# Performance work log

Hardware: AMD Instinct MI355X
Metric: run time of the kernel (lower is better)

## Reference

```python
import jax, jax.numpy as jnp
import numpy as np
import math

EPS = 1e-07
ITERATIONS = 3
FINAL_LAMBDA = 0.01

B, H, W, K, CIN, COUT, P = 8, 12, 12, 3, 16, 32, 16


def setup_inputs() -> dict:
    key = jax.random.key(0)
    k1, k2, k3, k4 = jax.random.split(key, 4)
    V = jax.random.normal(k1, (B, H, W, K, K, CIN, COUT, P), dtype=jnp.float32)
    a = jax.random.uniform(k2, (B, H, W, K, K, CIN, 1), dtype=jnp.float32)
    Beta_u = jax.random.normal(k3, (1, 1, 1, 1, 1, 1, COUT, 1), dtype=jnp.float32)
    Beta_a = jax.random.normal(k4, (1, 1, 1, 1, 1, 1, COUT), dtype=jnp.float32)
    R = jnp.full((B, H, W, K, K, CIN, COUT), 1.0 / COUT, dtype=jnp.float32)
    outSize = (B, H, W, COUT, P)
    return {"V": V, "a": a, "Beta_u": Beta_u, "Beta_a": Beta_a, "R": R, "outSize": outSize}


def _l2_normalize(x, axis):
    n = jnp.sqrt(jnp.sum(x * x, axis=axis, keepdims=True))
    return x / jnp.maximum(n, 1e-12)  # matches F.normalize default eps


def reference(V, a, Beta_u, Beta_a, R, outSize):
    mathpilog = jnp.log(jnp.asarray(2.0 * math.pi, dtype=jnp.float32))
    mu = sigma_sqr = a_out = None
    for i in range(ITERATIONS):
        Lam = FINAL_LAMBDA * (1.0 - 0.95 ** (i + 1))
        Rw = (R * a)[..., None]                                  # [B,h,w,K,K,Cin,Cout,1]
        mu_denom = jnp.sum(Rw, axis=(3, 4, 5), keepdims=True)    # [B,h,w,1,1,1,Cout,1]
        mu = jnp.sum(Rw * V, axis=(3, 4, 5), keepdims=True) / (mu_denom + EPS)  # [B,h,w,1,1,1,Cout,P]
        V_mu_sqr = (V - mu) ** 2                                 # [B,h,w,K,K,Cin,Cout,P]
        sigma_sqr = jnp.sum(Rw * V_mu_sqr, axis=(3, 4, 5), keepdims=True) / (mu_denom + EPS)
        cost_h = (Beta_u + 0.5 * jnp.log(sigma_sqr)) * mu_denom  # [B,h,w,1,1,1,Cout,P]
        x = Lam * (Beta_a - jnp.sum(cost_h, axis=7))             # [B,h,w,1,1,1,Cout]
        a_out = jax.nn.sigmoid(_l2_normalize(x, axis=6))
        log_p1 = -0.5 * jnp.sum(mathpilog + jnp.log(sigma_sqr), axis=7) + EPS
        log_p2 = -jnp.sum(V_mu_sqr / (2.0 * sigma_sqr + EPS), axis=7)  # [B,h,w,K,K,Cin,Cout]
        R = jax.nn.softmax(jnp.log(a_out) + log_p1 + log_p2, axis=6)
    mu_out = jnp.squeeze(mu).reshape(outSize)
    sigma_out = jnp.squeeze(sigma_sqr).reshape(outSize)
    return mu_out, jnp.squeeze(a_out), sigma_out
```

## Files before the change

### kernel.cpp

```cpp
#include <hip/hip_runtime.h>
#include <math.h>

#define NPOS 1152
#define NN   144
#define COUT 32
#define PP   16
#define EPSF 1e-7f
#define LOG2PI 1.8378770664093453f

#define MU_OFF   0
#define A_OFF    589824
#define SIG_OFF  626688

__global__ void __launch_bounds__(256)
em_routing_kernel(const float* __restrict__ V,
                  const float* __restrict__ a,
                  const float* __restrict__ Bu,
                  const float* __restrict__ Ba,
                  const float* __restrict__ Rin,
                  float* __restrict__ out)
{
    const int pos  = blockIdx.x;
    const int tid  = threadIdx.x;
    const int c    = tid & 31;
    const int slot = tid >> 5;
    const int wave = tid >> 6;

    const float* Vp = V + (size_t)pos * (NN * COUT * PP);
    const float* Rp = Rin + (size_t)pos * (NN * COUT);

    __shared__ float a_s[NN];
    __shared__ float red[4][COUT][33];
    __shared__ float fin[COUT][33];
    __shared__ float mu_s[COUT][17];
    __shared__ float wp_s[COUT][17];
    __shared__ float sg_s[COUT][17];
    __shared__ float cl_s[COUT];
    __shared__ float xs[COUT];
    __shared__ float sl_s[COUT];
    __shared__ float ao_s[COUT];
    __shared__ float nrm_s;

    for (int i = tid; i < NN; i += 256) a_s[i] = a[pos * NN + i];
    __syncthreads();

    const float lam_tab[3] = {0.01f * (1.f - 0.95f),
                              0.01f * (1.f - 0.95f * 0.95f),
                              0.01f * (1.f - 0.95f * 0.95f * 0.95f)};

    float mu_r[PP], wp_r[PP];
    float cl_r = 0.f;

    for (int it = 0; it < 3; ++it) {
        if (it > 0) {
            #pragma unroll
            for (int p = 0; p < PP; ++p) {
                mu_r[p] = mu_s[c][p];
                wp_r[p] = wp_s[c][p];
            }
            cl_r = cl_s[c];
        }

        float S0 = 0.f, S1[PP], S2[PP];
        #pragma unroll
        for (int p = 0; p < PP; ++p) { S1[p] = 0.f; S2[p] = 0.f; }

        for (int j = 0; j < 18; ++j) {
            const int n = slot + (j << 3);
            const float4* vp = (const float4*)(Vp + (size_t)n * (COUT * PP) + c * PP);
            float4 q0 = vp[0], q1 = vp[1], q2 = vp[2], q3 = vp[3];
            float v[PP] = {q0.x,q0.y,q0.z,q0.w, q1.x,q1.y,q1.z,q1.w,
                           q2.x,q2.y,q2.z,q2.w, q3.x,q3.y,q3.z,q3.w};
            float Rw;
            if (it == 0) {
                Rw = Rp[n * COUT + c] * a_s[n];
            } else {
                float acc = 0.f;
                #pragma unroll
                for (int p = 0; p < PP; ++p) {
                    float d = v[p] - mu_r[p];
                    acc = fmaf(d * wp_r[p], d, acc);
                }
                float logit = cl_r - acc;
                float m = logit;
                #pragma unroll
                for (int msk = 1; msk <= 16; msk <<= 1)
                    m = fmaxf(m, __shfl_xor(m, msk, 64));
                float e = __expf(logit - m);
                float sum = e;
                #pragma unroll
                for (int msk = 1; msk <= 16; msk <<= 1)
                    sum += __shfl_xor(sum, msk, 64);
                Rw = (e / sum) * a_s[n];
            }
            S0 += Rw;
            #pragma unroll
            for (int p = 0; p < PP; ++p) {
                float t = Rw * v[p];
                S1[p] += t;
                S2[p] = fmaf(t, v[p], S2[p]);
            }
        }

        S0 += __shfl_xor(S0, 32, 64);
        #pragma unroll
        for (int p = 0; p < PP; ++p) {
            S1[p] += __shfl_xor(S1[p], 32, 64);
            S2[p] += __shfl_xor(S2[p], 32, 64);
        }
        if ((tid & 32) == 0) {
            red[wave][c][0] = S0;
            #pragma unroll
            for (int p = 0; p < PP; ++p) {
                red[wave][c][1 + p]  = S1[p];
                red[wave][c][17 + p] = S2[p];
            }
        }
        __syncthreads();
        for (int idx = tid; idx < COUT * 33; idx += 256) {
            int cc = idx / 33, k = idx - cc * 33;
            fin[cc][k] = red[0][cc][k] + red[1][cc][k] + red[2][cc][k] + red[3][cc][k];
        }
        __syncthreads();

        if (tid < COUT) {
            const int cc = tid;
            float d0  = fin[cc][0];
            float inv = 1.f / (d0 + EPSF);
            float sumlog = 0.f;
            #pragma unroll
            for (int p = 0; p < PP; ++p) {
                float s1 = fin[cc][1 + p];
                float s2 = fin[cc][17 + p];
                float mu = s1 * inv;
                float sg = (s2 - 2.f * mu * s1 + mu * mu * d0) * inv;
                sg = fmaxf(sg, 1e-30f);
                mu_s[cc][p] = mu;
                sg_s[cc][p] = sg;
                wp_s[cc][p] = 1.f / (2.f * sg + EPSF);
                sumlog += logf(sg);
            }
            sl_s[cc] = sumlog;
            xs[cc] = lam_tab[it] * (Ba[cc] - d0 * (16.f * Bu[cc] + 0.5f * sumlog));
        }
        __syncthreads();
        if (tid == 0) {
            float nn2 = 0.f;
            for (int cc = 0; cc < COUT; ++cc) nn2 += xs[cc] * xs[cc];
            nrm_s = sqrtf(nn2);
        }
        __syncthreads();
        if (tid < COUT) {
            const int cc = tid;
            float y  = xs[cc] / fmaxf(nrm_s, 1e-12f);
            float ao = 1.f / (1.f + expf(-y));
            ao_s[cc] = ao;
            cl_s[cc] = logf(ao) + (-0.5f * (16.f * LOG2PI + sl_s[cc]) + EPSF);
        }
        __syncthreads();
    }

    for (int idx = tid; idx < COUT * PP; idx += 256) {
        int cc = idx >> 4, p = idx & 15;
        out[MU_OFF  + (size_t)pos * (COUT * PP) + idx] = mu_s[cc][p];
        out[SIG_OFF + (size_t)pos * (COUT * PP) + idx] = sg_s[cc][p];
    }
    if (tid < COUT) out[A_OFF + pos * COUT + tid] = ao_s[tid];
}

extern "C" void kernel_launch(void* const* d_in, const int* in_sizes, int n_in,
                              void* d_out, int out_size, void* d_ws, size_t ws_size,
                              hipStream_t stream) {
    const float* V  = (const float*)d_in[0];
    const float* a  = (const float*)d_in[1];
    const float* Bu = (const float*)d_in[2];
    const float* Ba = (const float*)d_in[3];
    const float* R  = (const float*)d_in[4];
    float* out = (float*)d_out;
    em_routing_kernel<<<NPOS, 256, 0, stream>>>(V, a, Bu, Ba, R, out);
}
```

Before: 572.0 us.

## Cache V as fp16 in workspace for later routing iterations

The first EM iteration reads fp32 V with nontemporal loads and also writes a packed fp16 copy into the workspace. Iterations two and three read that half-size copy instead of V, which halves their memory traffic. The finalize step replaces the single-thread norm with a wave shuffle reduction and drops two barriers. The fp16 rounding of V adds precision error in the later iterations, the first pass gains extra write traffic, and the fast path only runs when the workspace is large enough.

```diff
diff --git a/kernel.cpp b/kernel.cpp
--- a/kernel.cpp
+++ b/kernel.cpp
@@ -3,7 +3,7 @@
 
 #define NPOS 1152
 #define NN   144
-#define COUT 32
+#define COUTC 32
 #define PP   16
 #define EPSF 1e-7f
 #define LOG2PI 1.8378770664093453f
@@ -12,13 +12,28 @@
 #define A_OFF    589824
 #define SIG_OFF  626688
 
+typedef __attribute__((ext_vector_type(2))) __fp16    half2v;
+typedef __attribute__((ext_vector_type(4))) float     f32x4;
+typedef __attribute__((ext_vector_type(4))) unsigned  u32x4;
+
+static __device__ __forceinline__ unsigned pk2(float a, float b) {
+    half2v h = __builtin_amdgcn_cvt_pkrtz(a, b);
+    return __builtin_bit_cast(unsigned, h);
+}
+static __device__ __forceinline__ void unpk2(unsigned u, float& a, float& b) {
+    half2v h = __builtin_bit_cast(half2v, u);
+    a = (float)h.x; b = (float)h.y;
+}
+
+template<int USE_HALF>
 __global__ void __launch_bounds__(256)
 em_routing_kernel(const float* __restrict__ V,
                   const float* __restrict__ a,
                   const float* __restrict__ Bu,
                   const float* __restrict__ Ba,
                   const float* __restrict__ Rin,
-                  float* __restrict__ out)
+                  float* __restrict__ out,
+                  u32x4* __restrict__ Vh)
 {
     const int pos  = blockIdx.x;
     const int tid  = threadIdx.x;
@@ -26,20 +41,17 @@
     const int slot = tid >> 5;
     const int wave = tid >> 6;
 
-    const float* Vp = V + (size_t)pos * (NN * COUT * PP);
-    const float* Rp = Rin + (size_t)pos * (NN * COUT);
+    const float* Vp = V + (size_t)pos * (NN * COUTC * PP);
+    const float* Rp = Rin + (size_t)pos * (NN * COUTC);
 
     __shared__ float a_s[NN];
-    __shared__ float red[4][COUT][33];
-    __shared__ float fin[COUT][33];
-    __shared__ float mu_s[COUT][17];
-    __shared__ float wp_s[COUT][17];
-    __shared__ float sg_s[COUT][17];
-    __shared__ float cl_s[COUT];
-    __shared__ float xs[COUT];
-    __shared__ float sl_s[COUT];
-    __shared__ float ao_s[COUT];
-    __shared__ float nrm_s;
+    __shared__ float red[4][COUTC][33];
+    __shared__ float fin[COUTC][33];
+    __shared__ float mu_s[COUTC][17];
+    __shared__ float wp_s[COUTC][17];
+    __shared__ float sg_s[COUTC][17];
+    __shared__ float cl_s[COUTC];
+    __shared__ float ao_s[COUTC];
 
     for (int i = tid; i < NN; i += 256) a_s[i] = a[pos * NN + i];
     __syncthreads();
@@ -48,51 +60,85 @@
                               0.01f * (1.f - 0.95f * 0.95f),
                               0.01f * (1.f - 0.95f * 0.95f * 0.95f)};
 
-    float mu_r[PP], wp_r[PP];
-    float cl_r = 0.f;
-
-    for (int it = 0; it < 3; ++it) {
-        if (it > 0) {
-            #pragma unroll
-            for (int p = 0; p < PP; ++p) {
-                mu_r[p] = mu_s[c][p];
-                wp_r[p] = wp_s[c][p];
-            }
-            cl_r = cl_s[c];
-        }
-
+    auto reduce_finalize = [&](int it, float S0, float (&S1)[PP], float (&S2)[PP]) {
+        S0 += __shfl_xor(S0, 32, 64);
+        #pragma unroll
+        for (int p = 0; p < PP; ++p) {
+            S1[p] += __shfl_xor(S1[p], 32, 64);
+            S2[p] += __shfl_xor(S2[p], 32, 64);
+        }
+        if ((tid & 32) == 0) {
+            red[wave][c][0] = S0;
+            #pragma unroll
+            for (int p = 0; p < PP; ++p) {
+                red[wave][c][1 + p]  = S1[p];
+                red[wave][c][17 + p] = S2[p];
+            }
+        }
+        __syncthreads();
+        for (int idx = tid; idx < COUTC * 33; idx += 256) {
+            int cc = idx / 33, k = idx - cc * 33;
+            fin[cc][k] = red[0][cc][k] + red[1][cc][k] + red[2][cc][k] + red[3][cc][k];
+        }
+        __syncthreads();
+        if (tid < 64) {
+            float xv = 0.f, sumlog = 0.f;
+            if (tid < 32) {
+                const int cc = tid;
+                float d0  = fin[cc][0];
+                float inv = 1.f / (d0 + EPSF);
+                #pragma unroll
+                for (int p = 0; p < PP; ++p) {
+                    float s1 = fin[cc][1 + p];
+                    float s2 = fin[cc][17 + p];
+                    float mu = s1 * inv;
+                    float sg = (s2 - 2.f * mu * s1 + mu * mu * d0) * inv;
+                    sg = fmaxf(sg, 1e-30f);
+                    mu_s[cc][p] = mu;
+                    sg_s[cc][p] = sg;
+                    wp_s[cc][p] = 1.f / (2.f * sg + EPSF);
+                    sumlog += logf(sg);
+                }
+                xv = lam_tab[it] * (Ba[cc] - d0 * (16.f * Bu[cc] + 0.5f * sumlog));
+            }
+            float ss = xv * xv;
+            #pragma unroll
+            for (int m = 1; m <= 32; m <<= 1) ss += __shfl_xor(ss, m, 64);
+            if (tid < 32) {
+                float y  = xv / fmaxf(sqrtf(ss), 1e-12f);
+                float ao = 1.f / (1.f + expf(-y));
+                ao_s[tid] = ao;
+                cl_s[tid] = logf(ao) - 0.5f * (16.f * LOG2PI + sumlog) + EPSF;
+            }
+        }
+        __syncthreads();
+    };
+
+    {
         float S0 = 0.f, S1[PP], S2[PP];
         #pragma unroll
         for (int p = 0; p < PP; ++p) { S1[p] = 0.f; S2[p] = 0.f; }
 
+        #pragma unroll 3
         for (int j = 0; j < 18; ++j) {
             const int n = slot + (j << 3);
-            const float4* vp = (const float4*)(Vp + (size_t)n * (COUT * PP) + c * PP);
-            float4 q0 = vp[0], q1 = vp[1], q2 = vp[2], q3 = vp[3];
+            const f32x4* vp = (const f32x4*)(Vp + (size_t)n * (COUTC * PP) + c * PP);
+            f32x4 q0 = __builtin_nontemporal_load(vp);
+            f32x4 q1 = __builtin_nontemporal_load(vp + 1);
+            f32x4 q2 = __builtin_nontemporal_load(vp + 2);
+            f32x4 q3 = __builtin_nontemporal_load(vp + 3);
             float v[PP] = {q0.x,q0.y,q0.z,q0.w, q1.x,q1.y,q1.z,q1.w,
                            q2.x,q2.y,q2.z,q2.w, q3.x,q3.y,q3.z,q3.w};
-            float Rw;
-            if (it == 0) {
-                Rw = Rp[n * COUT + c] * a_s[n];
-            } else {
-                float acc = 0.f;
-                #pragma unroll
-                for (int p = 0; p < PP; ++p) {
-                    float d = v[p] - mu_r[p];
-                    acc = fmaf(d * wp_r[p], d, acc);
-                }
-                float logit = cl_r - acc;
-                float m = logit;
-                #pragma unroll
-                for (int msk = 1; msk <= 16; msk <<= 1)
-                    m = fmaxf(m, __shfl_xor(m, msk, 64));
-                float e = __expf(logit - m);
-                float sum = e;
-                #pragma unroll
-                for (int msk = 1; msk <= 16; msk <<= 1)
-                    sum += __shfl_xor(sum, msk, 64);
-                Rw = (e / sum) * a_s[n];
-            }
+            if (USE_HALF) {
+                size_t hb = ((size_t)(pos * NN + n) << 6) + (c << 1);
+                u32x4 u0, u1;
+                u0.x = pk2(v[0],  v[1]);  u0.y = pk2(v[2],  v[3]);
+                u0.z = pk2(v[4],  v[5]);  u0.w = pk2(v[6],  v[7]);
+                u1.x = pk2(v[8],  v[9]);  u1.y = pk2(v[10], v[11]);
+                u1.z = pk2(v[12], v[13]); u1.w = pk2(v[14], v[15]);
+                Vh[hb] = u0; Vh[hb + 1] = u1;
+            }
+            float Rw = __builtin_nontemporal_load(Rp + n * COUTC + c) * a_s[n];
             S0 += Rw;
             #pragma unroll
             for (int p = 0; p < PP; ++p) {
@@ -101,71 +147,75 @@
                 S2[p] = fmaf(t, v[p], S2[p]);
             }
         }
-
-        S0 += __shfl_xor(S0, 32, 64);
+        reduce_finalize(0, S0, S1, S2);
+    }
+
+    for (int it = 1; it < 3; ++it) {
+        float mu_r[PP], wp_r[PP];
+        #pragma unroll
+        for (int p = 0; p < PP; ++p) { mu_r[p] = mu_s[c][p]; wp_r[p] = wp_s[c][p]; }
+        float cl_r = cl_s[c];
         #pragma unroll
         for (int p = 0; p < PP; ++p) {
-            S1[p] += __shfl_xor(S1[p], 32, 64);
-            S2[p] += __shfl_xor(S2[p], 32, 64);
-        }
-        if ((tid & 32) == 0) {
-            red[wave][c][0] = S0;
-            #pragma unroll
-            for (int p = 0; p < PP; ++p) {
-                red[wave][c][1 + p]  = S1[p];
-                red[wave][c][17 + p] = S2[p];
-            }
-        }
-        __syncthreads();
-        for (int idx = tid; idx < COUT * 33; idx += 256) {
-            int cc = idx / 33, k = idx - cc * 33;
-            fin[cc][k] = red[0][cc][k] + red[1][cc][k] + red[2][cc][k] + red[3][cc][k];
-        }
-        __syncthreads();
-
-        if (tid < COUT) {
-            const int cc = tid;
-            float d0  = fin[cc][0];
-            float inv = 1.f / (d0 + EPSF);
-            float sumlog = 0.f;
-            #pragma unroll
-            for (int p = 0; p < PP; ++p) {
-                float s1 = fin[cc][1 + p];
-                float s2 = fin[cc][17 + p];
-                float mu = s1 * inv;
-                float sg = (s2 - 2.f * mu * s1 + mu * mu * d0) * inv;
-                sg = fmaxf(sg, 1e-30f);
-                mu_s[cc][p] = mu;
-                sg_s[cc][p] = sg;
-                wp_s[cc][p] = 1.f / (2.f * sg + EPSF);
-                sumlog += logf(sg);
-            }
-            sl_s[cc] = sumlog;
-            xs[cc] = lam_tab[it] * (Ba[cc] - d0 * (16.f * Bu[cc] + 0.5f * sumlog));
-        }
-        __syncthreads();
-        if (tid == 0) {
-            float nn2 = 0.f;
-            for (int cc = 0; cc < COUT; ++cc) nn2 += xs[cc] * xs[cc];
-            nrm_s = sqrtf(nn2);
-        }
-        __syncthreads();
-        if (tid < COUT) {
-            const int cc = tid;
-            float y  = xs[cc] / fmaxf(nrm_s, 1e-12f);
-            float ao = 1.f / (1.f + expf(-y));
-            ao_s[cc] = ao;
-            cl_s[cc] = logf(ao) + (-0.5f * (16.f * LOG2PI + sl_s[cc]) + EPSF);
-        }
-        __syncthreads();
-    }
-
-    for (int idx = tid; idx < COUT * PP; idx += 256) {
+            asm volatile("" : "+v"(mu_r[p]), "+v"(wp_r[p]));
+        }
+        asm volatile("" : "+v"(cl_r));
+
+        float S0 = 0.f, S1[PP], S2[PP];
+        #pragma unroll
+        for (int p = 0; p < PP; ++p) { S1[p] = 0.f; S2[p] = 0.f; }
+
+        for (int j = 0; j < 18; ++j) {
+            const int n = slot + (j << 3);
+            float v[PP];
+            if (USE_HALF) {
+                size_t hb = ((size_t)(pos * NN + n) << 6) + (c << 1);
+                u32x4 u0 = Vh[hb], u1 = Vh[hb + 1];
+                unsigned uu[8] = {u0.x, u0.y, u0.z, u0.w, u1.x, u1.y, u1.z, u1.w};
+                #pragma unroll
+                for (int k = 0; k < 8; ++k) unpk2(uu[k], v[2 * k], v[2 * k + 1]);
+            } else {
+                const f32x4* vp = (const f32x4*)(Vp + (size_t)n * (COUTC * PP) + c * PP);
+                f32x4 q0 = vp[0], q1 = vp[1], q2 = vp[2], q3 = vp[3];
+                v[0]=q0.x; v[1]=q0.y; v[2]=q0.z; v[3]=q0.w;
+                v[4]=q1.x; v[5]=q1.y; v[6]=q1.z; v[7]=q1.w;
+                v[8]=q2.x; v[9]=q2.y; v[10]=q2.z; v[11]=q2.w;
+                v[12]=q3.x; v[13]=q3.y; v[14]=q3.z; v[15]=q3.w;
+            }
+            float acc = 0.f;
+            #pragma unroll
+            for (int p = 0; p < PP; ++p) {
+                float d = v[p] - mu_r[p];
+                acc = fmaf(d * wp_r[p], d, acc);
+            }
+            float logit = cl_r - acc;
+            float m = logit;
+            #pragma unroll
+            for (int msk = 1; msk <= 16; msk <<= 1)
+                m = fmaxf(m, __shfl_xor(m, msk, 64));
+            float e = __expf(logit - m);
+            float sum = e;
+            #pragma unroll
+            for (int msk = 1; msk <= 16; msk <<= 1)
+                sum += __shfl_xor(sum, msk, 64);
+            float Rw = (e / sum) * a_s[n];
+            S0 += Rw;
+            #pragma unroll
+            for (int p = 0; p < PP; ++p) {
+                float t = Rw * v[p];
+                S1[p] += t;
+                S2[p] = fmaf(t, v[p], S2[p]);
+            }
+        }
+        reduce_finalize(it, S0, S1, S2);
+    }
+
+    for (int idx = tid; idx < COUTC * PP; idx += 256) {
         int cc = idx >> 4, p = idx & 15;
-        out[MU_OFF  + (size_t)pos * (COUT * PP) + idx] = mu_s[cc][p];
-        out[SIG_OFF + (size_t)pos * (COUT * PP) + idx] = sg_s[cc][p];
-    }
-    if (tid < COUT) out[A_OFF + pos * COUT + tid] = ao_s[tid];
+        out[MU_OFF  + (size_t)pos * (COUTC * PP) + idx] = mu_s[cc][p];
+        out[SIG_OFF + (size_t)pos * (COUTC * PP) + idx] = sg_s[cc][p];
+    }
+    if (tid < COUTC) out[A_OFF + pos * COUTC + tid] = ao_s[tid];
 }
 
 extern "C" void kernel_launch(void* const* d_in, const int* in_sizes, int n_in,
@@ -177,5 +227,10 @@
     const float* Ba = (const float*)d_in[3];
     const float* R  = (const float*)d_in[4];
     float* out = (float*)d_out;
-    em_routing_kernel<<<NPOS, 256, 0, stream>>>(V, a, Bu, Ba, R, out);
-}
+    const size_t need = (size_t)NPOS * NN * COUTC * PP * 2;
+    if (ws_size >= need) {
+        em_routing_kernel<1><<<NPOS, 256, 0, stream>>>(V, a, Bu, Ba, R, out, (u32x4*)d_ws);
+    } else {
+        em_routing_kernel<0><<<NPOS, 256, 0, stream>>>(V, a, Bu, Ba, R, out, (u32x4*)d_ws);
+    }
+}
```

Result: no change. 578.6 us (+1.2%).
